# Kernel tuning notes

Hardware: AMD Instinct MI355X
Metric: run time of the kernel (lower is better)

## Reference

```python
import jax, jax.numpy as jnp
import numpy as np

DIM = 64
HEADS = 8
NBLK = 4

def conv2d(x, w, b=None, groups=1, pad=0):
    out = jax.lax.conv_general_dilated(x, w, (1, 1), [(pad, pad), (pad, pad)],
        feature_group_count=groups, dimension_numbers=('NCHW', 'OIHW', 'NCHW'))
    return out if b is None else out + b[None, :, None, None]

def layer_norm_c(x, w, b):
    # WithBias LayerNorm over channel dim (torch code does it in (b,hw,c) layout)
    mu = jnp.mean(x, axis=1, keepdims=True)
    var = jnp.mean(jnp.square(x - mu), axis=1, keepdims=True)
    return (x - mu) / jnp.sqrt(var + 1e-5) * w[None, :, None, None] + b[None, :, None, None]

def l2norm(x):
    n = jnp.sqrt(jnp.sum(jnp.square(x), axis=-1, keepdims=True))
    return x / jnp.maximum(n, 1e-12)

def attention(x, w_qkv, w_dw, temp, w_proj):
    # transposed (channel) attention: C x C per head, N = h*w
    b, c, h, w = x.shape
    qkv = conv2d(conv2d(x, w_qkv), w_dw, groups=3 * c, pad=1)
    q, k, v = jnp.split(qkv, 3, axis=1)
    rs = lambda t: t.reshape(b, HEADS, c // HEADS, h * w)
    q, k, v = l2norm(rs(q)), l2norm(rs(k)), rs(v)
    attn = jax.nn.softmax(jnp.einsum('bhcn,bhdn->bhcd', q, k) * temp[None], axis=-1)
    out = jnp.einsum('bhcd,bhdn->bhcn', attn, v).reshape(b, c, h, w)
    return conv2d(out, w_proj)

def ffn(x, w_in, w_dw, w_out):
    y = conv2d(x, w_in)
    y = conv2d(y, w_dw, groups=y.shape[1], pad=1)
    y1, y2 = jnp.split(y, 2, axis=1)
    return conv2d(jax.nn.gelu(y1, approximate=False) * y2, w_out)

def ciim(low, high, w_ir, w_vi, w_fu, b_fu, w_dw, b_dw, eca_w):
    lf = conv2d(low, w_ir)   # [B, 2*DIM, H, W]
    hf = conv2d(high, w_vi)
    fuse = conv2d(jnp.concatenate([lf, hf], 1), w_fu, b_fu)  # [B, 2*DIM, H, W]
    la = jnp.broadcast_to(jnp.mean(lf, (2, 3), keepdims=True), lf.shape)
    ha = jnp.broadcast_to(jnp.mean(hf, (2, 3), keepdims=True), hf.shape)
    hl = conv2d(jnp.concatenate([fuse, la, ha], 1), w_dw, b_dw, groups=DIM, pad=1)  # 6*DIM -> DIM grouped
    h_map = jax.nn.sigmoid(jax.nn.gelu(hl, approximate=False))
    l_map = jax.nn.sigmoid(jax.nn.relu(hl))
    out = jnp.concatenate([h_map * low, l_map * high], 1)  # [B, 2*DIM, H, W]
    B, C, H, W = out.shape
    g = DIM // 2  # channel shuffle with groups = dim // 2
    out = out.reshape(B, g, C // g, H, W).swapaxes(1, 2).reshape(B, C, H, W)
    # eca_layer with k_size=1 reduces to per-channel sigmoid gate on the global mean
    y = jax.nn.sigmoid(jnp.mean(out, (2, 3)) * eca_w)
    return out * y[:, :, None, None]

def reference(inp_img, base_feature, detail_feature, w_conv_ir, w_conv_vi, w_conv_fusion,
              b_conv_fusion, w_dw_ciim, b_dw_ciim, eca_w, w_rc2, ln1_w, ln1_b, w_qkv,
              w_qkv_dw, temp, w_proj, ln2_w, ln2_b, w_in, w_ffn_dw, w_out_ffn, w_head1, w_head2):
    x0 = ciim(base_feature, detail_feature, w_conv_ir, w_conv_vi, w_conv_fusion,
              b_conv_fusion, w_dw_ciim, b_dw_ciim, eca_w)
    x0 = conv2d(x0, w_rc2)  # 2*DIM -> DIM
    x = x0
    for i in range(NBLK):
        x = x + attention(layer_norm_c(x, ln1_w[i], ln1_b[i]), w_qkv[i], w_qkv_dw[i], temp[i], w_proj[i])
        x = x + ffn(layer_norm_c(x, ln2_w[i], ln2_b[i]), w_in[i], w_ffn_dw[i], w_out_ffn[i])
    y = conv2d(x, w_head1, pad=1)
    y = jnp.where(y > 0, y, 0.01 * y)  # LeakyReLU(0.01)
    y = conv2d(y, w_head2, pad=1) + inp_img
    return jax.nn.sigmoid(y), x0

def setup_inputs():
    key = jax.random.key(0)
    ks = jax.random.split(key, 20)
    r = lambda k, s, sc=0.02: jax.random.normal(k, s, dtype=jnp.float32) * sc
    B, H, W = 4, 256, 256
    return {
        'inp_img': r(ks[0], (B, 1, H, W), 1.0),
        'base_feature': r(ks[1], (B, DIM, H, W), 1.0),
        'detail_feature': r(ks[2], (B, DIM, H, W), 1.0),
        'w_conv_ir': r(ks[3], (128, 64, 1, 1)),
        'w_conv_vi': r(ks[4], (128, 64, 1, 1)),
        'w_conv_fusion': r(ks[5], (128, 256, 1, 1)),
        'b_conv_fusion': jnp.zeros((128,), jnp.float32),
        'w_dw_ciim': r(ks[6], (64, 6, 3, 3)),
        'b_dw_ciim': jnp.zeros((64,), jnp.float32),
        'eca_w': r(ks[7], (128,), 1.0),
        'w_rc2': r(ks[8], (64, 128, 1, 1)),
        'ln1_w': jnp.ones((NBLK, 64), jnp.float32),
        'ln1_b': jnp.zeros((NBLK, 64), jnp.float32),
        'w_qkv': r(ks[9], (NBLK, 192, 64, 1, 1)),
        'w_qkv_dw': r(ks[10], (NBLK, 192, 1, 3, 3)),
        'temp': jnp.ones((NBLK, HEADS, 1, 1), jnp.float32),
        'w_proj': r(ks[11], (NBLK, 64, 64, 1, 1)),
        'ln2_w': jnp.ones((NBLK, 64), jnp.float32),
        'ln2_b': jnp.zeros((NBLK, 64), jnp.float32),
        'w_in': r(ks[12], (NBLK, 256, 64, 1, 1)),
        'w_ffn_dw': r(ks[13], (NBLK, 256, 1, 3, 3)),
        'w_out_ffn': r(ks[14], (NBLK, 64, 128, 1, 1)),
        'w_head1': r(ks[15], (32, 64, 3, 3)),
        'w_head2': r(ks[16], (1, 32, 3, 3)),
    }
```

## Files before the change

kernel.cpp:

```cpp
#include <hip/hip_runtime.h>
#include <hip/hip_bf16.h>
#include <math.h>

#define NP 65536L
#define HHH 256
#define WWW 256
#define QKCH 32

typedef unsigned short u16;
typedef unsigned short ushort8_t __attribute__((ext_vector_type(8)));
typedef short s16x8 __attribute__((ext_vector_type(8)));
typedef float f32x4 __attribute__((ext_vector_type(4)));

__device__ __forceinline__ float bf2f(u16 u) { return __uint_as_float(((unsigned)u) << 16); }
__device__ __forceinline__ u16 f2bf(float f) {
    __hip_bfloat16 h = __float2bfloat16(f);
    return *reinterpret_cast<u16*>(&h);
}
__device__ __forceinline__ float sigmoidf_(float x) { return 1.f / (1.f + __expf(-x)); }
__device__ __forceinline__ float gelu_exact(float x) {
    return 0.5f * x * (1.f + erff(x * 0.70710678118654752f));
}

__global__ void diag_kernel(float* out, float v) {
    if (threadIdx.x == 0 && blockIdx.x == 0) out[0] = v;
}

__global__ __launch_bounds__(256) void prep_misc(
    const float* __restrict__ wir, const float* __restrict__ wvi,
    const float* __restrict__ wfu, const float* __restrict__ wout,
    const float* __restrict__ wh1,
    u16* __restrict__ dir, u16* __restrict__ dvi,
    u16* __restrict__ dfu, u16* __restrict__ dout,
    u16* __restrict__ wtap)
{
    int bid = blockIdx.x;
    if (bid < 80) {
        long e = (long)bid * 1024 + threadIdx.x * 4;
        const float* src; u16* dst; long off;
        if (e < 8192)       { src = wir;  dst = dir;  off = 0; }
        else if (e < 16384) { src = wvi;  dst = dvi;  off = 8192; }
        else if (e < 49152) { src = wfu;  dst = dfu;  off = 16384; }
        else                { src = wout; dst = dout; off = 49152; }
        long i = e - off;
        float4 v = *(const float4*)(src + i);
        ushort4 o;
        o.x = f2bf(v.x); o.y = f2bf(v.y); o.z = f2bf(v.z); o.w = f2bf(v.w);
        *(ushort4*)(dst + i) = o;
    } else {
        int tap = bid - 80;
        for (int e = threadIdx.x; e < 2048; e += 256)
            wtap[tap * 2048 + e] = f2bf(wh1[(long)e * 9 + tap]);
    }
}

__global__ void fold_ln(
    const float* __restrict__ wqkv, const float* __restrict__ ln1w, const float* __restrict__ ln1b,
    const float* __restrict__ win,  const float* __restrict__ ln2w, const float* __restrict__ ln2b,
    u16* __restrict__ fq, float* __restrict__ fqB,
    u16* __restrict__ ff, float* __restrict__ ffB)
{
    int g = blockIdx.x;
    int i = g / 7, r = g % 7;
    const float *wsrc, *lg, *lb;
    u16* wd; float* Bd;
    int obase;
    if (r < 3) {
        wsrc = wqkv + (long)i * 192 * 64; lg = ln1w + i * 64; lb = ln1b + i * 64;
        wd = fq + (long)i * 192 * 64; Bd = fqB + i * 192; obase = r * 64;
    } else {
        wsrc = win + (long)i * 256 * 64; lg = ln2w + i * 64; lb = ln2b + i * 64;
        wd = ff + (long)i * 256 * 64; Bd = ffB + i * 256; obase = (r - 3) * 64;
    }
    int o = obase + threadIdx.x;
    float Bv = 0.f;
    for (int c = 0; c < 64; ++c) {
        float wv = wsrc[(long)o * 64 + c];
        wd[(long)o * 64 + c] = f2bf(wv * lg[c]);
        Bv += wv * lb[c];
    }
    Bd[o] = Bv;
}

__global__ __launch_bounds__(256) void gemm_irvi(
    const float* __restrict__ base, const float* __restrict__ detail,
    const u16* __restrict__ wir, const u16* __restrict__ wvi,
    u16* __restrict__ Y, float* __restrict__ means)
{
    __shared__ u16 XT[256][72];
    __shared__ u16 WT[64][72];
    __shared__ float red[4][64];
    int xsel = blockIdx.x, b = blockIdx.z;
    long P0 = (long)blockIdx.y * 256;
    int tid = threadIdx.x, lane = tid & 63, wave = tid >> 6;
    int rl = lane & 15, rg = lane >> 4;
    const float* in = ((xsel < 2) ? base : detail) + (long)b * 64 * NP;
    const u16* wsel = (xsel < 2) ? wir : wvi;
    int orow0 = (xsel & 1) * 64;
    int ochan0 = xsel * 64;

    {
        int o = tid >> 2, cs = (tid & 3) * 16;
        const u16* src = wsel + (long)(orow0 + o) * 64 + cs;
        *(ushort8_t*)&WT[o][cs] = *(const ushort8_t*)src;
        *(ushort8_t*)&WT[o][cs + 8] = *(const ushort8_t*)(src + 8);
    }
    {
        int c0 = (tid & 7) * 8;
        int pt = (tid >> 3) * 8;
        u16 rr[8][8];
#pragma unroll
        for (int i = 0; i < 8; ++i) {
            const float* sp = in + (long)(c0 + i) * NP + P0 + pt;
            float4 a = *(const float4*)sp;
            float4 b4 = *(const float4*)(sp + 4);
            rr[i][0] = f2bf(a.x); rr[i][1] = f2bf(a.y);
            rr[i][2] = f2bf(a.z); rr[i][3] = f2bf(a.w);
            rr[i][4] = f2bf(b4.x); rr[i][5] = f2bf(b4.y);
            rr[i][6] = f2bf(b4.z); rr[i][7] = f2bf(b4.w);
        }
#pragma unroll
        for (int j = 0; j < 8; ++j) {
            ushort8_t v;
#pragma unroll
            for (int i = 0; i < 8; ++i) v[i] = rr[i][j];
            *(ushort8_t*)&XT[pt + j][c0] = v;
        }
    }
    __syncthreads();
    f32x4 acc[4][4];
#pragma unroll
    for (int m = 0; m < 4; ++m)
#pragma unroll
        for (int n = 0; n < 4; ++n) acc[m][n] = (f32x4){0.f, 0.f, 0.f, 0.f};
#pragma unroll
    for (int ks = 0; ks < 2; ++ks) {
        int kc = ks * 32 + rg * 8;
        s16x8 a[4], bb[4];
#pragma unroll
        for (int m = 0; m < 4; ++m) a[m] = *(const s16x8*)&WT[m * 16 + rl][kc];
#pragma unroll
        for (int n = 0; n < 4; ++n) bb[n] = *(const s16x8*)&XT[wave * 64 + n * 16 + rl][kc];
#pragma unroll
        for (int m = 0; m < 4; ++m)
#pragma unroll
            for (int n = 0; n < 4; ++n)
                acc[m][n] = __builtin_amdgcn_mfma_f32_16x16x32_bf16(a[m], bb[n], acc[m][n], 0, 0, 0);
    }
    float csum[4][4];
#pragma unroll
    for (int m = 0; m < 4; ++m)
#pragma unroll
        for (int r = 0; r < 4; ++r) csum[m][r] = 0.f;
#pragma unroll
    for (int m = 0; m < 4; ++m)
#pragma unroll
        for (int n = 0; n < 4; ++n) {
            long px = P0 + wave * 64 + n * 16 + rl;
#pragma unroll
            for (int r = 0; r < 4; ++r) {
                int oo = ochan0 + m * 16 + rg * 4 + r;
                float v = acc[m][n][r];
                Y[((long)b * 256 + oo) * NP + px] = f2bf(v);
                csum[m][r] += v;
            }
        }
#pragma unroll
    for (int m = 0; m < 4; ++m)
#pragma unroll
        for (int r = 0; r < 4; ++r) {
            float s = csum[m][r];
            s += __shfl_xor(s, 1); s += __shfl_xor(s, 2);
            s += __shfl_xor(s, 4); s += __shfl_xor(s, 8);
            if (rl == 0) red[wave][m * 16 + rg * 4 + r] = s;
        }
    __syncthreads();
    if (tid < 64) {
        float v = red[0][tid] + red[1][tid] + red[2][tid] + red[3][tid];
        atomicAdd(&means[b * 256 + ochan0 + tid], v * (1.f / NP));
    }
}

__global__ __launch_bounds__(256) void gemm_plain(
    const u16* __restrict__ in, long inBS,
    const u16* __restrict__ wbf,
    const float* __restrict__ bias,
    u16* __restrict__ outp, long outBS, int Cin)
{
    __shared__ u16 XT[256][72];
    __shared__ u16 WT[64][72];
    int b = blockIdx.z;
    int oBase = blockIdx.x * 64;
    long P0 = (long)blockIdx.y * 256;
    int tid = threadIdx.x, lane = tid & 63, wave = tid >> 6;
    int rl = lane & 15, rg = lane >> 4;
    const u16* inB = in + (long)b * inBS;
    f32x4 acc[4][4];
#pragma unroll
    for (int m = 0; m < 4; ++m)
#pragma unroll
        for (int n = 0; n < 4; ++n) acc[m][n] = (f32x4){0.f, 0.f, 0.f, 0.f};
    for (int ck = 0; ck < Cin; ck += 64) {
        if (ck) __syncthreads();
        {
            int o = tid >> 2, cs = (tid & 3) * 16;
            const u16* src = wbf + (long)(oBase + o) * Cin + ck + cs;
            *(ushort8_t*)&WT[o][cs] = *(const ushort8_t*)src;
            *(ushort8_t*)&WT[o][cs + 8] = *(const ushort8_t*)(src + 8);
        }
        {
            int c0 = (tid & 7) * 8;
            int pt = (tid >> 3) * 8;
            ushort8_t r[8];
#pragma unroll
            for (int i = 0; i < 8; ++i)
                r[i] = *(const ushort8_t*)(inB + (long)(ck + c0 + i) * NP + P0 + pt);
#pragma unroll
            for (int j = 0; j < 8; ++j) {
                ushort8_t v;
#pragma unroll
                for (int i = 0; i < 8; ++i) v[i] = r[i][j];
                *(ushort8_t*)&XT[pt + j][c0] = v;
            }
        }
        __syncthreads();
#pragma unroll
        for (int ks = 0; ks < 2; ++ks) {
            int kc = ks * 32 + rg * 8;
            s16x8 a[4], bb[4];
#pragma unroll
            for (int m = 0; m < 4; ++m) a[m] = *(const s16x8*)&WT[m * 16 + rl][kc];
#pragma unroll
            for (int n = 0; n < 4; ++n) bb[n] = *(const s16x8*)&XT[wave * 64 + n * 16 + rl][kc];
#pragma unroll
            for (int m = 0; m < 4; ++m)
#pragma unroll
                for (int n = 0; n < 4; ++n)
                    acc[m][n] = __builtin_amdgcn_mfma_f32_16x16x32_bf16(a[m], bb[n], acc[m][n], 0, 0, 0);
        }
    }
#pragma unroll
    for (int m = 0; m < 4; ++m) {
#pragma unroll
        for (int n = 0; n < 4; ++n) {
            long px = P0 + wave * 64 + n * 16 + rl;
#pragma unroll
            for (int r = 0; r < 4; ++r) {
                int oo = oBase + m * 16 + rg * 4 + r;
                outp[(long)b * outBS + (long)oo * NP + px] = f2bf(acc[m][n][r] + bias[oo]);
            }
        }
    }
}

template<int WEFF, int RESID, int DUAL, int M2>
__global__ __launch_bounds__(256) void gemm_fused(
    const u16* __restrict__ in, long inBS,
    const u16* __restrict__ w1, long w1BS,
    const u16* __restrict__ residX,
    u16* __restrict__ Xout,
    float* __restrict__ out2,
    const u16* __restrict__ w2, const float* __restrict__ bias2,
    u16* __restrict__ Yout,
    const float* __restrict__ part, const float* __restrict__ temp,
    const float* __restrict__ wproj,
    int Cin)
{
    __shared__ u16 XT[128][72] __attribute__((aligned(16)));
    __shared__ u16 WT[64][72] __attribute__((aligned(16)));
    int b = blockIdx.z;
    long P0 = (long)blockIdx.x * 128;
    int tid = threadIdx.x, lane = tid & 63, wave = tid >> 6;
    int rl = lane & 15, rg = lane >> 4;
    const u16* inB = in + (long)b * inBS;

    if constexpr (WEFF) {
        float* SgF = (float*)&XT[0][0];
        float* attF = SgF + 640;
        for (int e = tid; e < 640; e += 256) {
            int h = e / 80, k = e % 80;
            const float* pp = part + (((long)b * 8 + h) * 80 + k) * QKCH;
            float s = 0.f;
#pragma unroll
            for (int c = 0; c < QKCH; ++c) s += pp[c];
            SgF[e] = s;
        }
        __syncthreads();
        if (tid < 64) {
            int h = tid >> 3, iq = tid & 7;
            float nqv = fmaxf(sqrtf(SgF[h * 80 + 64 + iq]), 1e-12f);
            float tp = temp[h];
            float row[8], mx = -1e30f;
#pragma unroll
            for (int jj = 0; jj < 8; ++jj) {
                float nkv = fmaxf(sqrtf(SgF[h * 80 + 72 + jj]), 1e-12f);
                row[jj] = SgF[h * 80 + iq * 8 + jj] / (nqv * nkv) * tp;
                mx = fmaxf(mx, row[jj]);
            }
            float sum = 0.f;
#pragma unroll
            for (int jj = 0; jj < 8; ++jj) { row[jj] = __expf(row[jj] - mx); sum += row[jj]; }
            float rinv = 1.f / sum;
#pragma unroll
            for (int jj = 0; jj < 8; ++jj) attF[(h * 8 + iq) * 8 + jj] = row[jj] * rinv;
        }
        __syncthreads();
        {
            int o = tid >> 2;
            int cv0 = (tid & 3) * 16;
#pragma unroll
            for (int cv = 0; cv < 16; ++cv) {
                int c = cv0 + cv;
                int h = c >> 3, jj = c & 7;
                float s = 0.f;
#pragma unroll
                for (int i = 0; i < 8; ++i)
                    s = fmaf(wproj[o * 64 + h * 8 + i], attF[(h * 8 + i) * 8 + jj], s);
                WT[o][c] = f2bf(s);
            }
        }
        __syncthreads();
    }

    f32x4 acc[4][2];
#pragma unroll
    for (int m = 0; m < 4; ++m)
#pragma unroll
        for (int n = 0; n < 2; ++n) acc[m][n] = (f32x4){0.f, 0.f, 0.f, 0.f};

    for (int ck = 0; ck < Cin; ck += 64) {
        if (ck) __syncthreads();
        if constexpr (!WEFF) {
            int o = tid >> 2, cs = (tid & 3) * 16;
            const u16* src = w1 + (long)b * w1BS + (long)o * Cin + ck + cs;
            *(ushort8_t*)&WT[o][cs] = *(const ushort8_t*)src;
            *(ushort8_t*)&WT[o][cs + 8] = *(const ushort8_t*)(src + 8);
        }
        if (tid < 128) {
            int c0 = (tid & 7) * 8;
            int pt = (tid >> 3) * 8;
            ushort8_t r[8];
#pragma unroll
            for (int i = 0; i < 8; ++i)
                r[i] = *(const ushort8_t*)(inB + (long)(ck + c0 + i) * NP + P0 + pt);
#pragma unroll
            for (int j = 0; j < 8; ++j) {
                ushort8_t v;
#pragma unroll
                for (int i = 0; i < 8; ++i) v[i] = r[i][j];
                *(ushort8_t*)&XT[pt + j][c0] = v;
            }
        }
        __syncthreads();
#pragma unroll
        for (int ks = 0; ks < 2; ++ks) {
            int kc = ks * 32 + rg * 8;
            s16x8 a[4], bb[2];
#pragma unroll
            for (int m = 0; m < 4; ++m) a[m] = *(const s16x8*)&WT[m * 16 + rl][kc];
#pragma unroll
            for (int n = 0; n < 2; ++n) bb[n] = *(const s16x8*)&XT[wave * 32 + n * 16 + rl][kc];
#pragma unroll
            for (int m = 0; m < 4; ++m)
#pragma unroll
                for (int n = 0; n < 2; ++n)
                    acc[m][n] = __builtin_amdgcn_mfma_f32_16x16x32_bf16(a[m], bb[n], acc[m][n], 0, 0, 0);
        }
    }

#pragma unroll
    for (int m = 0; m < 4; ++m)
#pragma unroll
        for (int n = 0; n < 2; ++n) {
            long px = P0 + wave * 32 + n * 16 + rl;
#pragma unroll
            for (int r = 0; r < 4; ++r) {
                int oo = m * 16 + rg * 4 + r;
                float t = acc[m][n][r];
                if constexpr (RESID) t += bf2f(residX[((long)b * 64 + oo) * NP + px]);
                acc[m][n][r] = t;
                Xout[((long)b * 64 + oo) * NP + px] = f2bf(t);
                if constexpr (DUAL) out2[((long)b * 64 + oo) * NP + px] = t;
            }
        }

    if constexpr (M2 > 0) {
        float muA[2], invA[2];
#pragma unroll
        for (int n = 0; n < 2; ++n) {
            float s = 0.f, s2 = 0.f;
#pragma unroll
            for (int m = 0; m < 4; ++m)
#pragma unroll
                for (int r = 0; r < 4; ++r) {
                    float t = acc[m][n][r];
                    s += t; s2 = fmaf(t, t, s2);
                }
            s += __shfl_xor(s, 16);  s += __shfl_xor(s, 32);
            s2 += __shfl_xor(s2, 16); s2 += __shfl_xor(s2, 32);
            float mu = s * (1.f / 64.f);
            float var = fmaxf(s2 * (1.f / 64.f) - mu * mu, 0.f);
            muA[n] = mu;
            invA[n] = rsqrtf(var + 1e-5f);
        }
        __syncthreads();
#pragma unroll
        for (int m = 0; m < 4; ++m)
#pragma unroll
            for (int n = 0; n < 2; ++n) {
                int pxl = wave * 32 + n * 16 + rl;
#pragma unroll
                for (int r = 0; r < 4; ++r)
                    XT[pxl][m * 16 + rg * 4 + r] = f2bf((acc[m][n][r] - muA[n]) * invA[n]);
            }
        __syncthreads();
        for (int mc = 0; mc < M2 / 64; ++mc) {
            if (mc) __syncthreads();
            {
                int o = tid >> 2, cs = (tid & 3) * 16;
                const u16* src = w2 + (long)(mc * 64 + o) * 64 + cs;
                *(ushort8_t*)&WT[o][cs] = *(const ushort8_t*)src;
                *(ushort8_t*)&WT[o][cs + 8] = *(const ushort8_t*)(src + 8);
            }
            __syncthreads();
            f32x4 a2[4][2];
#pragma unroll
            for (int m = 0; m < 4; ++m)
#pragma unroll
                for (int n = 0; n < 2; ++n) a2[m][n] = (f32x4){0.f, 0.f, 0.f, 0.f};
#pragma unroll
            for (int ks = 0; ks < 2; ++ks) {
                int kc = ks * 32 + rg * 8;
                s16x8 a[4], bb[2];
#pragma unroll
                for (int m = 0; m < 4; ++m) a[m] = *(const s16x8*)&WT[m * 16 + rl][kc];
#pragma unroll
                for (int n = 0; n < 2; ++n) bb[n] = *(const s16x8*)&XT[wave * 32 + n * 16 + rl][kc];
#pragma unroll
                for (int m = 0; m < 4; ++m)
#pragma unroll
                    for (int n = 0; n < 2; ++n)
                        a2[m][n] = __builtin_amdgcn_mfma_f32_16x16x32_bf16(a[m], bb[n], a2[m][n], 0, 0, 0);
            }
#pragma unroll
            for (int m = 0; m < 4; ++m) {
#pragma unroll
                for (int n = 0; n < 2; ++n) {
                    long px = P0 + wave * 32 + n * 16 + rl;
#pragma unroll
                    for (int r = 0; r < 4; ++r) {
                        int oo = mc * 64 + m * 16 + rg * 4 + r;
                        Yout[((long)b * 256 + oo) * NP + px] = f2bf(a2[m][n][r] + bias2[oo]);
                    }
                }
            }
        }
    }
}

__device__ __forceinline__ void stage_row(float (*S)[260], const u16* __restrict__ src,
                                          int y0, int j, int px)
{
    int row = y0 - 1 + j;
    if (row >= 0 && row < HHH) {
        ushort8_t a = *(const ushort8_t*)(src + row * WWW + px);
        ushort8_t b = *(const ushort8_t*)(src + row * WWW + px + 8);
#pragma unroll
        for (int e = 0; e < 8; ++e) { S[j][1 + px + e] = bf2f(a[e]); S[j][9 + px + e] = bf2f(b[e]); }
    } else {
#pragma unroll
        for (int e = 0; e < 16; ++e) S[j][1 + px + e] = 0.f;
    }
}
__device__ __forceinline__ float conv9(const float (*S)[260], int r, int col,
                                       const float* __restrict__ w9)
{
    float a = 0.f;
#pragma unroll
    for (int ky = 0; ky < 3; ++ky)
#pragma unroll
        for (int kx = 0; kx < 3; ++kx)
            a = fmaf(w9[ky * 3 + kx], S[r + ky][col + kx], a);
    return a;
}

__global__ __launch_bounds__(256) void dw3x3_strip(
    const u16* __restrict__ in, long inBS, const float* __restrict__ w,
    u16* __restrict__ out1, long out1BS,
    u16* __restrict__ out2, long out2BS, int obase2, int csplit)
{
    int strip = blockIdx.x, c = blockIdx.y, b = blockIdx.z;
    int y0 = strip * 16, tid = threadIdx.x;
    __shared__ float S[18][260];
    const u16* src = in + (long)b * inBS + (long)c * NP;
    int j = tid >> 4, px = (tid & 15) * 16;
    stage_row(S, src, y0, j, px);
    if (tid < 32) stage_row(S, src, y0, 16 + (tid >> 4), px);
    if (tid < 18) { S[tid][0] = 0.f; S[tid][257] = 0.f; }
    __syncthreads();
    float w9[9];
#pragma unroll
    for (int k = 0; k < 9; ++k) w9[k] = w[c * 9 + k];
    u16* dst = (c < csplit)
                   ? out1 + (long)b * out1BS + (long)c * NP
                   : out2 + (long)b * out2BS + (long)(obase2 + c - csplit) * NP;
    int px4 = (tid & 63) * 4;
    int r0 = (tid >> 6) * 4;
#pragma unroll
    for (int r = 0; r < 4; ++r) {
        int row = r0 + r;
        ushort4 ovec;
        u16* ov = (u16*)&ovec;
#pragma unroll
        for (int e = 0; e < 4; ++e) ov[e] = f2bf(conv9(S, row, px4 + e, w9));
        *(ushort4*)&dst[(y0 + row) * WWW + px4] = ovec;
    }
}

__global__ __launch_bounds__(256) void ffn_dw_glu_strip(
    const u16* __restrict__ y, long yBS, const float* __restrict__ w,
    u16* __restrict__ g, long gBS)
{
    int strip = blockIdx.x, c = blockIdx.y, b = blockIdx.z;
    int y0 = strip * 16, tid = threadIdx.x;
    __shared__ float S1[18][260];
    __shared__ float S2[18][260];
    const u16* s1 = y + (long)b * yBS + (long)c * NP;
    const u16* s2 = y + (long)b * yBS + (long)(c + 128) * NP;
    int j = tid >> 4, px = (tid & 15) * 16;
    stage_row(S1, s1, y0, j, px);
    if (tid < 32) stage_row(S1, s1, y0, 16 + (tid >> 4), px);
    stage_row(S2, s2, y0, j, px);
    if (tid < 32) stage_row(S2, s2, y0, 16 + (tid >> 4), px);
    if (tid < 18) { S1[tid][0] = S1[tid][257] = 0.f; S2[tid][0] = S2[tid][257] = 0.f; }
    __syncthreads();
    float w1[9], w2[9];
#pragma unroll
    for (int k = 0; k < 9; ++k) { w1[k] = w[c * 9 + k]; w2[k] = w[(c + 128) * 9 + k]; }
    u16* dst = g + (long)b * gBS + (long)c * NP;
    int px4 = (tid & 63) * 4;
    int r0 = (tid >> 6) * 4;
#pragma unroll
    for (int r = 0; r < 4; ++r) {
        int row = r0 + r;
        ushort4 ovec;
        u16* ov = (u16*)&ovec;
#pragma unroll
        for (int e = 0; e < 4; ++e) {
            float a1 = conv9(S1, row, px4 + e, w1);
            float a2 = conv9(S2, row, px4 + e, w2);
            ov[e] = f2bf(gelu_exact(a1) * a2);
        }
        *(ushort4*)&dst[(y0 + row) * WWW + px4] = ovec;
    }
}

__global__ __launch_bounds__(256) void ciim_dw_strip(
    const u16* __restrict__ fuse, long fBS, const float* __restrict__ means,
    const float* __restrict__ wdw, const float* __restrict__ bdw,
    u16* __restrict__ hl, long hlBS)
{
    int strip = blockIdx.x, c = blockIdx.y, b = blockIdx.z;
    int y0 = strip * 16, tid = threadIdx.x;
    __shared__ float S[18][260];
    int px4 = (tid & 63) * 4;
    int r0 = (tid >> 6) * 4;
    float acc[4][4];
    float bias = bdw[c];
#pragma unroll
    for (int r = 0; r < 4; ++r)
#pragma unroll
        for (int e = 0; e < 4; ++e) acc[r][e] = bias;
    for (int j6 = 0; j6 < 6; ++j6) {
        int ic = 6 * c + j6;
        const float* w9p = wdw + (c * 6 + j6) * 9;
        float w9[9];
#pragma unroll
        for (int k = 0; k < 9; ++k) w9[k] = w9p[k];
        if (ic < 128) {
            __syncthreads();
            const u16* src = fuse + (long)b * fBS + (long)ic * NP;
            int j = tid >> 4, px = (tid & 15) * 16;
            stage_row(S, src, y0, j, px);
            if (tid < 32) stage_row(S, src, y0, 16 + (tid >> 4), px);
            if (tid < 18) { S[tid][0] = 0.f; S[tid][257] = 0.f; }
            __syncthreads();
#pragma unroll
            for (int r = 0; r < 4; ++r)
#pragma unroll
                for (int e = 0; e < 4; ++e) acc[r][e] += conv9(S, r0 + r, px4 + e, w9);
        } else {
            float mv = means[b * 256 + ic - 128];
#pragma unroll
            for (int r = 0; r < 4; ++r) {
                int row = y0 + r0 + r;
#pragma unroll
                for (int e = 0; e < 4; ++e) {
                    int xc = px4 + e;
                    float ws = 0.f;
#pragma unroll
                    for (int ky = 0; ky < 3; ++ky) {
                        int yy = row + ky - 1;
                        if (yy < 0 || yy >= HHH) continue;
#pragma unroll
                        for (int kx = 0; kx < 3; ++kx) {
                            int xx = xc + kx - 1;
                            if (xx < 0 || xx >= WWW) continue;
                            ws += w9[ky * 3 + kx];
                        }
                    }
                    acc[r][e] += mv * ws;
                }
            }
        }
    }
    u16* dst = hl + (long)b * hlBS + (long)c * NP;
#pragma unroll
    for (int r = 0; r < 4; ++r) {
        ushort4 ovec;
        u16* ov = (u16*)&ovec;
#pragma unroll
        for (int e = 0; e < 4; ++e) ov[e] = f2bf(acc[r][e]);
        *(ushort4*)&dst[(y0 + r0 + r) * WWW + px4] = ovec;
    }
}

__global__ __launch_bounds__(256) void outsh4(
    const u16* __restrict__ hl, long hlBS,
    const float* __restrict__ low, long lBS,
    const float* __restrict__ high,
    u16* __restrict__ outb, long oBS,
    float* __restrict__ ecam)
{
    long p = ((long)blockIdx.x * 256 + threadIdx.x) * 4;
    int cn = blockIdx.y, b = blockIdx.z;
    int co = (cn & 31) * 4 + (cn >> 5);
    const u16* hp;
    const float* sp;
    if (co < 64) {
        hp = hl + (long)b * hlBS + (long)co * NP + p;
        sp = low + (long)b * lBS + (long)co * NP + p;
    } else {
        hp = hl + (long)b * hlBS + (long)(co - 64) * NP + p;
        sp = high + (long)b * lBS + (long)(co - 64) * NP + p;
    }
    ushort4 hu = *(const ushort4*)hp;
    float4 sv = *(const float4*)sp;
    float hv[4] = {bf2f(hu.x), bf2f(hu.y), bf2f(hu.z), bf2f(hu.w)};
    float s4[4] = {sv.x, sv.y, sv.z, sv.w};
    ushort4 ovec;
    u16* ov = (u16*)&ovec;
    float psum = 0.f;
#pragma unroll
    for (int k = 0; k < 4; ++k) {
        float gg = (co < 64) ? sigmoidf_(gelu_exact(hv[k])) : sigmoidf_(fmaxf(hv[k], 0.f));
        float val = gg * s4[k];
        ov[k] = f2bf(val);
        psum += val;
    }
    *(ushort4*)((u16*)outb + (long)b * oBS + (long)cn * NP + p) = ovec;
    __shared__ float red[256];
    red[threadIdx.x] = psum;
    __syncthreads();
    for (int st = 128; st > 0; st >>= 1) {
        if (threadIdx.x < st) red[threadIdx.x] += red[threadIdx.x + st];
        __syncthreads();
    }
    if (threadIdx.x == 0) atomicAdd(&ecam[b * 128 + cn], red[0] * (1.f / NP));
}

__global__ __launch_bounds__(256) void rc2w_build(
    const float* __restrict__ ecam, const float* __restrict__ ecaw,
    const float* __restrict__ wrc2, u16* __restrict__ wout)
{
    int idx = blockIdx.x * 256 + threadIdx.x;
    int c = idx & 127, o = (idx >> 7) & 63, b = idx >> 13;
    float y = sigmoidf_(ecam[b * 128 + c] * ecaw[c]);
    wout[idx] = f2bf(wrc2[o * 128 + c] * y);
}

__global__ __launch_bounds__(256) void qk_dot(
    const u16* __restrict__ D, long dBS, float* __restrict__ part)
{
    int chunk = blockIdx.x, h = blockIdx.y, b = blockIdx.z;
    int tid = threadIdx.x, lane = tid & 63, wave = tid >> 6;
    const u16* q = D + (long)b * dBS + (long)(h * 8) * NP;
    const u16* k = q + 64 * NP;
    float dots[64], nq[8], nk[8];
#pragma unroll
    for (int a = 0; a < 64; ++a) dots[a] = 0.f;
#pragma unroll
    for (int a = 0; a < 8; ++a) { nq[a] = 0.f; nk[a] = 0.f; }
    long p = (long)chunk * 2048 + tid * 8;
    {
        ushort8_t qv[8], kv[8];
#pragma unroll
        for (int i = 0; i < 8; ++i) qv[i] = *(const ushort8_t*)(q + (long)i * NP + p);
#pragma unroll
        for (int i = 0; i < 8; ++i) kv[i] = *(const ushort8_t*)(k + (long)i * NP + p);
#pragma unroll
        for (int e = 0; e < 8; ++e) {
            float qe[8], ke[8];
#pragma unroll
            for (int i = 0; i < 8; ++i) { qe[i] = bf2f(qv[i][e]); ke[i] = bf2f(kv[i][e]); }
#pragma unroll
            for (int i = 0; i < 8; ++i) {
                nq[i] = fmaf(qe[i], qe[i], nq[i]);
                nk[i] = fmaf(ke[i], ke[i], nk[i]);
#pragma unroll
                for (int jj = 0; jj < 8; ++jj)
                    dots[i * 8 + jj] = fmaf(qe[i], ke[jj], dots[i * 8 + jj]);
            }
        }
    }
    __shared__ float red[4][80];
#pragma unroll
    for (int a = 0; a < 64; ++a) {
        float v = dots[a];
#pragma unroll
        for (int o = 32; o > 0; o >>= 1) v += __shfl_xor(v, o);
        if (lane == 0) red[wave][a] = v;
    }
#pragma unroll
    for (int a = 0; a < 8; ++a) {
        float v1 = nq[a], v2 = nk[a];
#pragma unroll
        for (int o = 32; o > 0; o >>= 1) { v1 += __shfl_xor(v1, o); v2 += __shfl_xor(v2, o); }
        if (lane == 0) { red[wave][64 + a] = v1; red[wave][72 + a] = v2; }
    }
    __syncthreads();
    if (tid < 80) {
        float v = red[0][tid] + red[1][tid] + red[2][tid] + red[3][tid];
        part[(((long)b * 8 + h) * 80 + tid) * QKCH + chunk] = v;
    }
}

__global__ __launch_bounds__(256) void head_fused(
    const u16* __restrict__ X, const u16* __restrict__ wtap,
    const float* __restrict__ wh2, const float* __restrict__ inp,
    float* __restrict__ out)
{
    __shared__ u16 P[18][18][72] __attribute__((aligned(16)));
    __shared__ u16 Hl[16][16][40] __attribute__((aligned(16)));
    __shared__ float w2t[288];
    int ty = blockIdx.x, tx = blockIdx.y, b = blockIdx.z;
    int tid = threadIdx.x, lane = tid & 63, wave = tid >> 6;
    int rl = lane & 15, rg = lane >> 4;
    int oy = ty * 14 - 2, ox = tx * 14 - 2;
    for (int idx = tid; idx < 288; idx += 256)
        w2t[(idx % 9) * 32 + idx / 9] = wh2[idx];
    {
        int lane5 = tid & 31;
        int cbase = tid >> 5;
#pragma unroll
        for (int cg = 0; cg < 8; ++cg) {
            int c = cg * 8 + cbase;
            const u16* src = X + ((long)b * 64 + c) * NP;
            for (int it = 0; it < 11; ++it) {
                int px = lane5 + it * 32;
                if (px < 324) {
                    int row = px / 18, col = px % 18;
                    int gy = oy + row, gx = ox + col;
                    u16 v = (gy >= 0 && gy < HHH && gx >= 0 && gx < WWW)
                                ? src[gy * WWW + gx] : (u16)0;
                    P[row][col][c] = v;
                }
            }
        }
    }
    __syncthreads();
    f32x4 acc[2][4];
#pragma unroll
    for (int m = 0; m < 2; ++m)
#pragma unroll
        for (int n = 0; n < 4; ++n) acc[m][n] = (f32x4){0.f, 0.f, 0.f, 0.f};
#pragma unroll
    for (int tap = 0; tap < 9; ++tap) {
        int ky = tap / 3, kx = tap % 3;
#pragma unroll
        for (int ks = 0; ks < 2; ++ks) {
            int kc = ks * 32 + rg * 8;
            s16x8 a0 = *(const s16x8*)(wtap + tap * 2048 + (long)(0 + rl) * 64 + kc);
            s16x8 a1 = *(const s16x8*)(wtap + tap * 2048 + (long)(16 + rl) * 64 + kc);
#pragma unroll
            for (int n = 0; n < 4; ++n) {
                int py = wave * 4 + n;
                s16x8 bb = *(const s16x8*)&P[py + ky][kx + rl][kc];
                acc[0][n] = __builtin_amdgcn_mfma_f32_16x16x32_bf16(a0, bb, acc[0][n], 0, 0, 0);
                acc[1][n] = __builtin_amdgcn_mfma_f32_16x16x32_bf16(a1, bb, acc[1][n], 0, 0, 0);
            }
        }
    }
#pragma unroll
    for (int m = 0; m < 2; ++m)
#pragma unroll
        for (int n = 0; n < 4; ++n) {
            int py = wave * 4 + n;
            int gy = ty * 14 - 1 + py, gx = tx * 14 - 1 + rl;
            bool ok = (gy >= 0 && gy < HHH && gx >= 0 && gx < WWW);
#pragma unroll
            for (int r = 0; r < 4; ++r) {
                int o = m * 16 + rg * 4 + r;
                float v = acc[m][n][r];
                v = v > 0.f ? v : 0.01f * v;
                Hl[py][rl][o] = ok ? f2bf(v) : (u16)0;
            }
        }
    __syncthreads();
    if (tid < 196) {
        int r = tid / 14, c = tid % 14;
        int gy = ty * 14 + r, gx = tx * 14 + c;
        if (gy < HHH && gx < WWW) {
            float acc2 = 0.f;
#pragma unroll
            for (int tap = 0; tap < 9; ++tap) {
                int hy = r + tap / 3, hx = c + tap % 3;
#pragma unroll
                for (int cg = 0; cg < 4; ++cg) {
                    ushort8_t hv = *(const ushort8_t*)&Hl[hy][hx][cg * 8];
#pragma unroll
                    for (int e = 0; e < 8; ++e)
                        acc2 = fmaf(w2t[tap * 32 + cg * 8 + e], bf2f(hv[e]), acc2);
                }
            }
            float v = acc2 + inp[(long)b * NP + gy * WWW + gx];
            out[(long)b * NP + gy * WWW + gx] = 1.f / (1.f + expf(-v));
        }
    }
}

extern "C" void kernel_launch(void* const* d_in, const int* in_sizes, int n_in,
                              void* d_out, int out_size, void* d_ws, size_t ws_size,
                              hipStream_t stream)
{
    const float* inp    = (const float*)d_in[0];
    const float* base   = (const float*)d_in[1];
    const float* detail = (const float*)d_in[2];
    const float* w_ir   = (const float*)d_in[3];
    const float* w_vi   = (const float*)d_in[4];
    const float* w_fu   = (const float*)d_in[5];
    const float* b_fu   = (const float*)d_in[6];
    const float* w_dwc  = (const float*)d_in[7];
    const float* b_dwc  = (const float*)d_in[8];
    const float* eca_w  = (const float*)d_in[9];
    const float* w_rc2  = (const float*)d_in[10];
    const float* ln1w   = (const float*)d_in[11];
    const float* ln1b   = (const float*)d_in[12];
    const float* w_qkv  = (const float*)d_in[13];
    const float* w_qdw  = (const float*)d_in[14];
    const float* temp   = (const float*)d_in[15];
    const float* w_proj = (const float*)d_in[16];
    const float* ln2w   = (const float*)d_in[17];
    const float* ln2b   = (const float*)d_in[18];
    const float* w_in_  = (const float*)d_in[19];
    const float* w_fdw  = (const float*)d_in[20];
    const float* w_out_ = (const float*)d_in[21];
    const float* w_h1   = (const float*)d_in[22];
    const float* w_h2   = (const float*)d_in[23];

    float* out = (float*)d_out;

    auto needB = [&](long nb) -> size_t {
        return (size_t)nb * NP * (64 * 2 + 256 * 2 + 128 * 2) + (4u << 20);
    };
    int bInner;
    if (ws_size >= needB(4)) bInner = 4;
    else if (ws_size >= needB(2)) bInner = 2;
    else if (ws_size >= needB(1)) bInner = 1;
    else {
        diag_kernel<<<1, 64, 0, stream>>>(out, (float)(ws_size >> 20));
        return;
    }
    const long nb = bInner;

    char* p = (char*)d_ws;
    auto alloc = [&](size_t bytes) -> char* {
        char* r = p; p += (bytes + 255) & ~(size_t)255; return r;
    };
    u16*   X      = (u16*)alloc((size_t)nb * 64 * NP * 2);
    u16*   Y      = (u16*)alloc((size_t)nb * 256 * NP * 2);
    u16*   Dq     = (u16*)alloc((size_t)nb * 128 * NP * 2);
    float* part   = (float*)alloc((size_t)nb * 8 * 80 * QKCH * 4);
    float* means  = (float*)alloc((size_t)nb * 384 * 4);
    float* ecam   = means + nb * 256;
    u16*   rc2wb  = (u16*)alloc((size_t)nb * 8192 * 2);
    u16*   fq_bf  = (u16*)alloc((size_t)4 * 192 * 64 * 2);
    float* fqB    = (float*)alloc((size_t)4 * 192 * 4);
    u16*   ff_bf  = (u16*)alloc((size_t)4 * 256 * 64 * 2);
    float* ffB    = (float*)alloc((size_t)4 * 256 * 4);
    u16*   wir_bf = (u16*)alloc(8192 * 2);
    u16*   wvi_bf = (u16*)alloc(8192 * 2);
    u16*   wfu_bf = (u16*)alloc(32768 * 2);
    u16*   wout_bf= (u16*)alloc(32768 * 2);
    u16*   wtap   = (u16*)alloc(9 * 2048 * 2);

    dim3 blk(256);

    fold_ln<<<dim3(28), dim3(64), 0, stream>>>(w_qkv, ln1w, ln1b, w_in_, ln2w, ln2b,
                                               fq_bf, fqB, ff_bf, ffB);
    prep_misc<<<dim3(89), blk, 0, stream>>>(w_ir, w_vi, w_fu, w_out_, w_h1,
                                            wir_bf, wvi_bf, wfu_bf, wout_bf, wtap);

    for (int b0 = 0; b0 < 4; b0 += bInner) {
        const float* inpB    = inp + (long)b0 * NP;
        const float* baseB   = base + (long)b0 * 64 * NP;
        const float* detailB = detail + (long)b0 * 64 * NP;
        float* out0  = out + (long)b0 * NP;
        float* outX0 = out + 262144 + (long)b0 * 64 * NP;

        hipMemsetAsync(means, 0, (size_t)nb * 384 * 4, stream);
        gemm_irvi<<<dim3(4, 256, nb), blk, 0, stream>>>(
            baseB, detailB, wir_bf, wvi_bf, Y, means);
        gemm_plain<<<dim3(2, 256, nb), blk, 0, stream>>>(
            Y, 256 * NP, wfu_bf, b_fu, Dq, 128 * NP, 256);
        ciim_dw_strip<<<dim3(16, 64, nb), blk, 0, stream>>>(
            Dq, 128 * NP, means, w_dwc, b_dwc, Y + 128 * NP, 256 * NP);
        outsh4<<<dim3(64, 128, nb), blk, 0, stream>>>(
            Y + 128 * NP, 256 * NP, baseB, 64 * NP, detailB, Y, 256 * NP, ecam);
        rc2w_build<<<dim3(nb * 32), blk, 0, stream>>>(ecam, eca_w, w_rc2, rc2wb);
        gemm_fused<0, 0, 1, 192><<<dim3(512, 1, nb), blk, 0, stream>>>(
            Y, 256 * NP, rc2wb, 8192, nullptr, X, outX0,
            fq_bf, fqB, Y, nullptr, nullptr, nullptr, 128);

        for (int i = 0; i < 4; ++i) {
            dw3x3_strip<<<dim3(16, 192, nb), blk, 0, stream>>>(
                Y, 256 * NP, w_qdw + (long)i * 192 * 9,
                Dq, 128 * NP, Y, 256 * NP, 192, 128);
            qk_dot<<<dim3(QKCH, 8, nb), blk, 0, stream>>>(Dq, 128 * NP, part);
            gemm_fused<1, 1, 0, 256><<<dim3(512, 1, nb), blk, 0, stream>>>(
                Y + 192 * NP, 256 * NP, nullptr, 0, X, X, nullptr,
                ff_bf + (long)i * 256 * 64, ffB + i * 256, Y,
                part, temp + i * 8, w_proj + (long)i * 4096, 64);
            ffn_dw_glu_strip<<<dim3(16, 128, nb), blk, 0, stream>>>(
                Y, 256 * NP, w_fdw + (long)i * 256 * 9, Dq, 128 * NP);
            if (i < 3) {
                gemm_fused<0, 1, 0, 192><<<dim3(512, 1, nb), blk, 0, stream>>>(
                    Dq, 128 * NP, wout_bf + (long)i * 8192, 0, X, X, nullptr,
                    fq_bf + (long)(i + 1) * 192 * 64, fqB + (i + 1) * 192, Y,
                    nullptr, nullptr, nullptr, 128);
            } else {
                gemm_fused<0, 1, 0, 0><<<dim3(512, 1, nb), blk, 0, stream>>>(
                    Dq, 128 * NP, wout_bf + (long)i * 8192, 0, X, X, nullptr,
                    nullptr, nullptr, nullptr, nullptr, nullptr, nullptr, 128);
            }
        }

        head_fused<<<dim3(19, 19, nb), blk, 0, stream>>>(X, wtap, w_h2, inpB, out0);
    }
}
```

Before: 1.761 ms.

## Fuse CIIM gating into depthwise kernel and emit pixel-major X for head

```diff
diff --git a/kernel.cpp b/kernel.cpp
--- a/kernel.cpp
+++ b/kernel.cpp
@@ -253,7 +253,7 @@
     }
 }
 
-template<int WEFF, int RESID, int DUAL, int M2>
+template<int WEFF, int RESID, int DUAL, int M2, int PIXMAJ>
 __global__ __launch_bounds__(256) void gemm_fused(
     const u16* __restrict__ in, long inBS,
     const u16* __restrict__ w1, long w1BS,
@@ -379,10 +379,30 @@
                 float t = acc[m][n][r];
                 if constexpr (RESID) t += bf2f(residX[((long)b * 64 + oo) * NP + px]);
                 acc[m][n][r] = t;
-                Xout[((long)b * 64 + oo) * NP + px] = f2bf(t);
+                if constexpr (!PIXMAJ) Xout[((long)b * 64 + oo) * NP + px] = f2bf(t);
                 if constexpr (DUAL) out2[((long)b * 64 + oo) * NP + px] = t;
             }
         }
+
+    if constexpr (PIXMAJ) {
+        __syncthreads();
+#pragma unroll
+        for (int m = 0; m < 4; ++m)
+#pragma unroll
+            for (int n = 0; n < 2; ++n) {
+                int pxl = wave * 32 + n * 16 + rl;
+#pragma unroll
+                for (int r = 0; r < 4; ++r)
+                    XT[pxl][m * 16 + rg * 4 + r] = f2bf(acc[m][n][r]);
+            }
+        __syncthreads();
+        int pxl = tid >> 1, c0 = (tid & 1) * 32;
+        u16* dst = Xout + (long)b * (64 * NP) + (P0 + pxl) * 64 + c0;
+        *(ushort8_t*)(dst)      = *(const ushort8_t*)&XT[pxl][c0];
+        *(ushort8_t*)(dst + 8)  = *(const ushort8_t*)&XT[pxl][c0 + 8];
+        *(ushort8_t*)(dst + 16) = *(const ushort8_t*)&XT[pxl][c0 + 16];
+        *(ushort8_t*)(dst + 24) = *(const ushort8_t*)&XT[pxl][c0 + 24];
+    }
 
     if constexpr (M2 > 0) {
         float muA[2], invA[2];
@@ -555,10 +575,11 @@
     }
 }
 
-__global__ __launch_bounds__(256) void ciim_dw_strip(
+__global__ __launch_bounds__(256) void ciim_dw_gate(
     const u16* __restrict__ fuse, long fBS, const float* __restrict__ means,
     const float* __restrict__ wdw, const float* __restrict__ bdw,
-    u16* __restrict__ hl, long hlBS)
+    const float* __restrict__ low, long lBS, const float* __restrict__ high,
+    u16* __restrict__ Yout, long yBS, float* __restrict__ ecam)
 {
     int strip = blockIdx.x, c = blockIdx.y, b = blockIdx.z;
     int y0 = strip * 16, tid = threadIdx.x;
@@ -614,59 +635,46 @@
             }
         }
     }
-    u16* dst = hl + (long)b * hlBS + (long)c * NP;
+    int cn1 = 32 * (c & 3) + (c >> 2);
+    int cn2 = cn1 + 16;
+    u16* d1 = Yout + (long)b * yBS + (long)cn1 * NP;
+    u16* d2 = Yout + (long)b * yBS + (long)cn2 * NP;
+    const float* lp = low + (long)b * lBS + (long)c * NP;
+    const float* hp = high + (long)b * lBS + (long)c * NP;
+    float s1 = 0.f, s2 = 0.f;
 #pragma unroll
     for (int r = 0; r < 4; ++r) {
-        ushort4 ovec;
-        u16* ov = (u16*)&ovec;
-#pragma unroll
-        for (int e = 0; e < 4; ++e) ov[e] = f2bf(acc[r][e]);
-        *(ushort4*)&dst[(y0 + r0 + r) * WWW + px4] = ovec;
-    }
-}
-
-__global__ __launch_bounds__(256) void outsh4(
-    const u16* __restrict__ hl, long hlBS,
-    const float* __restrict__ low, long lBS,
-    const float* __restrict__ high,
-    u16* __restrict__ outb, long oBS,
-    float* __restrict__ ecam)
-{
-    long p = ((long)blockIdx.x * 256 + threadIdx.x) * 4;
-    int cn = blockIdx.y, b = blockIdx.z;
-    int co = (cn & 31) * 4 + (cn >> 5);
-    const u16* hp;
-    const float* sp;
-    if (co < 64) {
-        hp = hl + (long)b * hlBS + (long)co * NP + p;
-        sp = low + (long)b * lBS + (long)co * NP + p;
-    } else {
-        hp = hl + (long)b * hlBS + (long)(co - 64) * NP + p;
-        sp = high + (long)b * lBS + (long)(co - 64) * NP + p;
-    }
-    ushort4 hu = *(const ushort4*)hp;
-    float4 sv = *(const float4*)sp;
-    float hv[4] = {bf2f(hu.x), bf2f(hu.y), bf2f(hu.z), bf2f(hu.w)};
-    float s4[4] = {sv.x, sv.y, sv.z, sv.w};
-    ushort4 ovec;
-    u16* ov = (u16*)&ovec;
-    float psum = 0.f;
-#pragma unroll
-    for (int k = 0; k < 4; ++k) {
-        float gg = (co < 64) ? sigmoidf_(gelu_exact(hv[k])) : sigmoidf_(fmaxf(hv[k], 0.f));
-        float val = gg * s4[k];
-        ov[k] = f2bf(val);
-        psum += val;
-    }
-    *(ushort4*)((u16*)outb + (long)b * oBS + (long)cn * NP + p) = ovec;
-    __shared__ float red[256];
-    red[threadIdx.x] = psum;
+        int row = y0 + r0 + r;
+        float4 lv = *(const float4*)(lp + row * WWW + px4);
+        float4 hv = *(const float4*)(hp + row * WWW + px4);
+        float l4[4] = {lv.x, lv.y, lv.z, lv.w};
+        float h4[4] = {hv.x, hv.y, hv.z, hv.w};
+        ushort4 o1, o2;
+        u16* p1 = (u16*)&o1;
+        u16* p2 = (u16*)&o2;
+#pragma unroll
+        for (int e = 0; e < 4; ++e) {
+            float hl = acc[r][e];
+            float v1 = sigmoidf_(gelu_exact(hl)) * l4[e];
+            float v2 = sigmoidf_(fmaxf(hl, 0.f)) * h4[e];
+            p1[e] = f2bf(v1); p2[e] = f2bf(v2);
+            s1 += v1; s2 += v2;
+        }
+        *(ushort4*)&d1[row * WWW + px4] = o1;
+        *(ushort4*)&d2[row * WWW + px4] = o2;
+    }
+    __syncthreads();
+    float* redbuf = &S[0][0];
+    redbuf[tid] = s1; redbuf[256 + tid] = s2;
     __syncthreads();
     for (int st = 128; st > 0; st >>= 1) {
-        if (threadIdx.x < st) red[threadIdx.x] += red[threadIdx.x + st];
+        if (tid < st) { redbuf[tid] += redbuf[tid + st]; redbuf[256 + tid] += redbuf[256 + tid + st]; }
         __syncthreads();
     }
-    if (threadIdx.x == 0) atomicAdd(&ecam[b * 128 + cn], red[0] * (1.f / NP));
+    if (tid == 0) {
+        atomicAdd(&ecam[b * 128 + cn1], redbuf[0] * (1.f / NP));
+        atomicAdd(&ecam[b * 128 + cn2], redbuf[256] * (1.f / NP));
+    }
 }
 
 __global__ __launch_bounds__(256) void rc2w_build(
@@ -736,7 +744,7 @@
 }
 
 __global__ __launch_bounds__(256) void head_fused(
-    const u16* __restrict__ X, const u16* __restrict__ wtap,
+    const u16* __restrict__ Xp, const u16* __restrict__ wtap,
     const float* __restrict__ wh2, const float* __restrict__ inp,
     float* __restrict__ out)
 {
@@ -750,22 +758,17 @@
     for (int idx = tid; idx < 288; idx += 256)
         w2t[(idx % 9) * 32 + idx / 9] = wh2[idx];
     {
-        int lane5 = tid & 31;
-        int cbase = tid >> 5;
-#pragma unroll
-        for (int cg = 0; cg < 8; ++cg) {
-            int c = cg * 8 + cbase;
-            const u16* src = X + ((long)b * 64 + c) * NP;
-            for (int it = 0; it < 11; ++it) {
-                int px = lane5 + it * 32;
-                if (px < 324) {
-                    int row = px / 18, col = px % 18;
-                    int gy = oy + row, gx = ox + col;
-                    u16 v = (gy >= 0 && gy < HHH && gx >= 0 && gx < WWW)
-                                ? src[gy * WWW + gx] : (u16)0;
-                    P[row][col][c] = v;
-                }
-            }
+        const u16* xb = Xp + (long)b * (64 * NP);
+        int c0 = (tid & 7) * 8;
+        for (int pp = tid >> 3; pp < 324; pp += 32) {
+            int row = pp / 18, col = pp % 18;
+            int gy = oy + row, gx = ox + col;
+            ushort8_t v;
+            if (gy >= 0 && gy < HHH && gx >= 0 && gx < WWW)
+                v = *(const ushort8_t*)(xb + ((long)(gy * WWW + gx)) * 64 + c0);
+            else
+                v = (ushort8_t){0, 0, 0, 0, 0, 0, 0, 0};
+            *(ushort8_t*)&P[row][col][c0] = v;
         }
     }
     __syncthreads();
@@ -913,12 +916,11 @@
             baseB, detailB, wir_bf, wvi_bf, Y, means);
         gemm_plain<<<dim3(2, 256, nb), blk, 0, stream>>>(
             Y, 256 * NP, wfu_bf, b_fu, Dq, 128 * NP, 256);
-        ciim_dw_strip<<<dim3(16, 64, nb), blk, 0, stream>>>(
-            Dq, 128 * NP, means, w_dwc, b_dwc, Y + 128 * NP, 256 * NP);
-        outsh4<<<dim3(64, 128, nb), blk, 0, stream>>>(
-            Y + 128 * NP, 256 * NP, baseB, 64 * NP, detailB, Y, 256 * NP, ecam);
+        ciim_dw_gate<<<dim3(16, 64, nb), blk, 0, stream>>>(
+            Dq, 128 * NP, means, w_dwc, b_dwc, baseB, 64 * NP, detailB,
+            Y, 256 * NP, ecam);
         rc2w_build<<<dim3(nb * 32), blk, 0, stream>>>(ecam, eca_w, w_rc2, rc2wb);
-        gemm_fused<0, 0, 1, 192><<<dim3(512, 1, nb), blk, 0, stream>>>(
+        gemm_fused<0, 0, 1, 192, 0><<<dim3(512, 1, nb), blk, 0, stream>>>(
             Y, 256 * NP, rc2wb, 8192, nullptr, X, outX0,
             fq_bf, fqB, Y, nullptr, nullptr, nullptr, 128);
 
@@ -927,24 +929,24 @@
                 Y, 256 * NP, w_qdw + (long)i * 192 * 9,
                 Dq, 128 * NP, Y, 256 * NP, 192, 128);
             qk_dot<<<dim3(QKCH, 8, nb), blk, 0, stream>>>(Dq, 128 * NP, part);
-            gemm_fused<1, 1, 0, 256><<<dim3(512, 1, nb), blk, 0, stream>>>(
+            gemm_fused<1, 1, 0, 256, 0><<<dim3(512, 1, nb), blk, 0, stream>>>(
                 Y + 192 * NP, 256 * NP, nullptr, 0, X, X, nullptr,
                 ff_bf + (long)i * 256 * 64, ffB + i * 256, Y,
                 part, temp + i * 8, w_proj + (long)i * 4096, 64);
             ffn_dw_glu_strip<<<dim3(16, 128, nb), blk, 0, stream>>>(
                 Y, 256 * NP, w_fdw + (long)i * 256 * 9, Dq, 128 * NP);
             if (i < 3) {
-                gemm_fused<0, 1, 0, 192><<<dim3(512, 1, nb), blk, 0, stream>>>(
+                gemm_fused<0, 1, 0, 192, 0><<<dim3(512, 1, nb), blk, 0, stream>>>(
                     Dq, 128 * NP, wout_bf + (long)i * 8192, 0, X, X, nullptr,
                     fq_bf + (long)(i + 1) * 192 * 64, fqB + (i + 1) * 192, Y,
                     nullptr, nullptr, nullptr, 128);
             } else {
-                gemm_fused<0, 1, 0, 0><<<dim3(512, 1, nb), blk, 0, stream>>>(
-                    Dq, 128 * NP, wout_bf + (long)i * 8192, 0, X, X, nullptr,
+                gemm_fused<0, 1, 0, 0, 1><<<dim3(512, 1, nb), blk, 0, stream>>>(
+                    Dq, 128 * NP, wout_bf + (long)i * 8192, 0, X, Y, nullptr,
                     nullptr, nullptr, nullptr, nullptr, nullptr, nullptr, 128);
             }
         }
 
-        head_fused<<<dim3(19, 19, nb), blk, 0, stream>>>(X, wtap, w_h2, inpB, out0);
-    }
-}
+        head_fused<<<dim3(19, 19, nb), blk, 0, stream>>>(Y, wtap, w_h2, inpB, out0);
+    }
+}
```

New measurement: 1.636 ms. -7.1%, faster.
